# Performance work log

Hardware: AMD Instinct MI355X
Metric: run time of the kernel (lower is better)

Reference implementation:

```python
import jax, jax.numpy as jnp
import numpy as np

D = 512
H = 4
HD = D // H
FF = 4 * D
B = 512
T = 128
EMA_K = 128
LOC_K = 4
DECAY = 0.9
STEP = 0.5 / np.sqrt(128 / 32)  # 0.25
EPS = 1e-5


def layernorm(x, g, b):
    mu = jnp.mean(x, axis=-1, keepdims=True)
    var = jnp.mean(jnp.square(x - mu), axis=-1, keepdims=True)
    return (x - mu) * jax.lax.rsqrt(var + EPS) * g + b


def dwconv_causal(x, w):
    # x: (B,T,D), w: (D,K); torch Conv1d(groups=D, padding=K-1) sliced to [:T]
    K = w.shape[1]
    xt = jnp.transpose(x, (0, 2, 1))  # (B,D,T)
    y = jax.lax.conv_general_dilated(
        xt, w[:, None, :], window_strides=(1,), padding=[(K - 1, 0)],
        feature_group_count=x.shape[-1], dimension_numbers=('NCT', 'OIT', 'NCT'))
    return jnp.transpose(y, (0, 2, 1))


def rope(qk, cos, sin):
    # qk: (B,H,T,HD)
    x1, x2 = jnp.split(qk, 2, axis=-1)
    rot = jnp.concatenate([-x2, x1], axis=-1)
    return qk * cos + rot * sin


def setup_inputs() -> dict:
    key = jax.random.key(0)
    ks = jax.random.split(key, 24)
    s = 0.02
    inp = {
        'parallel_repr': jax.random.normal(ks[0], (B, T, D), jnp.float32),
        'sequential_state': jax.random.normal(ks[1], (B, D), jnp.float32),
        'q_w': jax.random.normal(ks[2], (D, D), jnp.float32) * s,
        'q_b': jnp.zeros((D,), jnp.float32),
        'k_w': jax.random.normal(ks[3], (D, D), jnp.float32) * s,
        'k_b': jnp.zeros((D,), jnp.float32),
        'v_w': jax.random.normal(ks[4], (D, D), jnp.float32) * s,
        'v_b': jnp.zeros((D,), jnp.float32),
        'o_w': jax.random.normal(ks[5], (D, D), jnp.float32) * s,
        'o_b': jnp.zeros((D,), jnp.float32),
        'local_w': jax.random.normal(ks[6], (D, LOC_K), jnp.float32) * 0.1,
        'local_b': jax.random.normal(ks[7], (D,), jnp.float32) * 0.1,
        'delta_w': jax.random.normal(ks[8], (3 * D, D), jnp.float32) * s,
        'delta_b': jnp.zeros((D,), jnp.float32),
        'gate_w': jax.random.normal(ks[9], (3 * D, D), jnp.float32) * s,
        'gate_b': jnp.zeros((D,), jnp.float32),
        'dn_g': jnp.ones((D,), jnp.float32), 'dn_b': jnp.zeros((D,), jnp.float32),
        'ln1_g': jnp.ones((D,), jnp.float32), 'ln1_b': jnp.zeros((D,), jnp.float32),
        'ln2_g': jnp.ones((D,), jnp.float32), 'ln2_b': jnp.zeros((D,), jnp.float32),
        'ln3_g': jnp.ones((D,), jnp.float32), 'ln3_b': jnp.zeros((D,), jnp.float32),
        'ln4_g': jnp.ones((D,), jnp.float32), 'ln4_b': jnp.zeros((D,), jnp.float32),
        'seq_w': jax.random.normal(ks[10], (D, D), jnp.float32) * s,
        'seq_b': jnp.zeros((D,), jnp.float32),
        'ffn_w1': jax.random.normal(ks[11], (D, FF), jnp.float32) * s,
        'ffn_b1': jnp.zeros((FF,), jnp.float32),
        'ffn_w2': jax.random.normal(ks[12], (FF, D), jnp.float32) * s,
        'ffn_b2': jnp.zeros((D,), jnp.float32),
    }
    # EMA kernel: coefficient (1-d)*d^lag on x[t-lag]; stored flipped as in torch
    ema = (1.0 - DECAY) * DECAY ** jnp.arange(EMA_K, dtype=jnp.float32)
    inp['ema_w'] = jnp.broadcast_to(ema[::-1][None, :], (D, EMA_K))
    return inp


def reference(parallel_repr, sequential_state, q_w, q_b, k_w, k_b, v_w, v_b,
              o_w, o_b, local_w, local_b, delta_w, delta_b, gate_w, gate_b,
              dn_g, dn_b, ln1_g, ln1_b, ln2_g, ln2_b, ln3_g, ln3_b, ln4_g, ln4_b,
              seq_w, seq_b, ffn_w1, ffn_b1, ffn_w2, ffn_b2, ema_w):
    x = parallel_repr
    Bb, Tt, Dd = x.shape
    # --- RoPE causal attention ---
    inv_freq = 1.0 / (10000.0 ** (jnp.arange(0, HD, 2, dtype=jnp.float32) / HD))
    t = jnp.arange(Tt, dtype=jnp.float32)
    freqs = jnp.outer(t, inv_freq)                      # (T, HD/2)
    emb = jnp.concatenate([freqs, freqs], axis=-1)      # (T, HD)
    cos = jnp.cos(emb)[None, None]
    sin = jnp.sin(emb)[None, None]
    def heads(y):
        return jnp.transpose(y.reshape(Bb, Tt, H, HD), (0, 2, 1, 3))
    q = rope(heads(x @ q_w + q_b), cos, sin)
    k = rope(heads(x @ k_w + k_b), cos, sin)
    v = heads(x @ v_w + v_b)
    scores = jnp.einsum('bhtd,bhsd->bhts', q, k) / np.sqrt(HD)
    causal = jnp.tril(jnp.ones((Tt, Tt), dtype=bool))
    scores = jnp.where(causal, scores, jnp.float32(-1e9))
    attn = jax.nn.softmax(scores, axis=-1)
    attn_out = jnp.einsum('bhts,bhsd->bhtd', attn, v)
    attn_out = jnp.transpose(attn_out, (0, 2, 1, 3)).reshape(Bb, Tt, Dd)
    attn_out = attn_out @ o_w + o_b
    x1 = layernorm(x + attn_out, ln1_g, ln1_b)
    # --- depthwise causal convs ---
    local_hist = dwconv_causal(x1, local_w) + local_b
    global_sum = dwconv_causal(x1, ema_w)
    combined = jnp.concatenate([x1, local_hist, global_sum], axis=-1)  # (B,T,3D)
    deltas = jax.nn.sigmoid(combined @ gate_w + gate_b) * jnp.tanh(combined @ delta_w + delta_b)
    deltas = layernorm(deltas, dn_g, dn_b)
    acc = jnp.cumsum(deltas, axis=1) * STEP
    states = layernorm(sequential_state[:, None, :] + acc, ln3_g, ln3_b)
    seq_guidance = states @ seq_w + seq_b
    ffn_in = x1 + 0.3 * seq_guidance
    h = jax.nn.gelu(ffn_in @ ffn_w1 + ffn_b1, approximate=False)
    ffn_out = h @ ffn_w2 + ffn_b2
    out = layernorm(x1 + ffn_out, ln2_g, ln2_b)
    final_state = layernorm(states[:, -1, :], ln4_g, ln4_b)
    return out, final_state
```

## Files before the change

### kernel.cpp

```cpp
#include <hip/hip_runtime.h>
#include <cstddef>
#include <cstdint>

#define BB   512
#define TT   128
#define DD   512
#define HH   4
#define HDIM 128
#define FFD  2048
#define NROWS (BB * TT)
#define SLOT ((size_t)NROWS * DD)

typedef unsigned short u16;
typedef __bf16 bf16x8 __attribute__((ext_vector_type(8)));
typedef float  f32x4  __attribute__((ext_vector_type(4)));

__device__ __forceinline__ u16 f2b(float x) {
    union { float f; unsigned u; } v; v.f = x;
    unsigned r = v.u + 0x7FFFu + ((v.u >> 16) & 1u);
    return (u16)(r >> 16);
}
__device__ __forceinline__ float b2f(u16 u) {
    union { unsigned u; float f; } v; v.u = (unsigned)u << 16; return v.f;
}
__device__ __forceinline__ float fast_gelu(float v) {
    float t = v * (0.7978845608028654f + 0.0356774081f * v * v);
    float e = __expf(2.f * t);
    float th = 1.f - 2.f / (e + 1.f);
    return 0.5f * v * (1.f + th);
}
__device__ __forceinline__ void glds16(const void* g, void* l) {
    __builtin_amdgcn_global_load_lds(
        (const __attribute__((address_space(1))) void*)g,
        (__attribute__((address_space(3))) void*)l, 16, 0, 0);
}

#define BAR() asm volatile("s_barrier" ::: "memory")
#define MM(ACC, AV, BV) \
    ACC = __builtin_amdgcn_mfma_f32_16x16x32_bf16(AV, BV, ACC, 0, 0, 0)

template<int MODE>
__global__ __launch_bounds__(512, 2)
void gemm256(const u16* __restrict__ A, const u16* __restrict__ BT,
             const float* __restrict__ bias, void* __restrict__ Cout, int ldc,
             const float* __restrict__ addsrc, int K, int M)
{
    __shared__ u16 S[65536];
    const int tid = threadIdx.x;
    const int gx  = gridDim.x;
    const int nwg = gx * gridDim.y;
    int orig = blockIdx.y * gx + blockIdx.x;
    orig = (orig & 7) * (nwg >> 3) + (orig >> 3);
    const int row0 = (orig / gx) * 256;
    const int col0 = (orig % gx) * 256;

    const int lane = tid & 63;
    const int wid  = tid >> 6;
    const int wm   = wid >> 2;
    const int wn   = wid & 3;
    const int fr   = lane & 15;
    const int kq   = lane >> 4;

    const int c0 = wid * 128 + lane;
    const int c1 = c0 + 64;
    const int l0 = c0 ^ (((c0 >> 5) & 1) << 1);
    const int l1 = c1 ^ (((c1 >> 5) & 1) << 1);
    const int sr0 = l0 >> 2, sk0 = (l0 & 3) * 8;
    const int sr1 = l1 >> 2, sk1 = (l1 & 3) * 8;
    const u16* ApG = A  + (size_t)row0 * K;
    const u16* BpG = BT + (size_t)col0 * K;

    auto stA = [&](int kt, int kh) {
        char* slot = (char*)S + ((((kt & 1) << 1) + kh) << 14);
        const u16* g = ApG + kt * 64 + kh * 32;
        glds16(g + (size_t)sr0 * K + sk0, slot + c0 * 16);
        glds16(g + (size_t)sr1 * K + sk1, slot + c1 * 16);
    };
    auto stB = [&](int kt, int kh) {
        char* slot = (char*)S + 65536 + ((((kt & 1) << 1) + kh) << 14);
        const u16* g = BpG + kt * 64 + kh * 32;
        glds16(g + (size_t)sr0 * K + sk0, slot + c0 * 16);
        glds16(g + (size_t)sr1 * K + sk1, slot + c1 * 16);
    };
    auto rdA = [&](int p, int kh, int m) -> bf16x8 {
        const int row = wm * 128 + m * 16 + fr;
        const int L = (row * 64 + kq * 16) ^ (((row >> 3) & 1) << 5);
        return *(const bf16x8*)((char*)S + (((p << 1) + kh) << 14) + L);
    };
    auto rdB = [&](int p, int kh, int n) -> bf16x8 {
        const int col = wn * 64 + n * 16 + fr;
        const int L = (col * 64 + kq * 16) ^ (((col >> 3) & 1) << 5);
        return *(const bf16x8*)((char*)S + 65536 + (((p << 1) + kh) << 14) + L);
    };

    f32x4 acc[8][4];
#pragma unroll
    for (int m = 0; m < 8; ++m)
#pragma unroll
        for (int n = 0; n < 4; ++n) acc[m][n] = (f32x4){0.f, 0.f, 0.f, 0.f};

    const int NKT = K >> 6;

    stA(0, 0); stA(0, 1); stB(0, 0); stB(0, 1);
    stB(1, 0); stB(1, 1); stA(1, 0);
    asm volatile("s_waitcnt vmcnt(6)" ::: "memory");
    BAR();

    for (int kt = 0; kt < NKT; ++kt) {
        const int p = kt & 1;
        const bool s1 = (kt + 1 < NKT);
        const bool s2 = (kt + 2 < NKT);
        bf16x8 a0, a1, a2, a3, a4, a5, a6, a7;
        bf16x8 b00, b01, b02, b03, b10, b11, b12, b13;

        if (s1) stA(kt + 1, 1);
        a0 = rdA(p, 0, 0); a1 = rdA(p, 0, 1); a2 = rdA(p, 0, 2); a3 = rdA(p, 0, 3);
        a4 = rdA(p, 1, 0); a5 = rdA(p, 1, 1); a6 = rdA(p, 1, 2); a7 = rdA(p, 1, 3);
        b00 = rdB(p, 0, 0); b01 = rdB(p, 0, 1);
        b10 = rdB(p, 1, 0); b11 = rdB(p, 1, 1);
        BAR();
        __builtin_amdgcn_s_setprio(1);
        MM(acc[0][0], a0, b00); MM(acc[0][1], a0, b01);
        MM(acc[1][0], a1, b00); MM(acc[1][1], a1, b01);
        MM(acc[2][0], a2, b00); MM(acc[2][1], a2, b01);
        MM(acc[3][0], a3, b00); MM(acc[3][1], a3, b01);
        MM(acc[0][0], a4, b10); MM(acc[0][1], a4, b11);
        MM(acc[1][0], a5, b10); MM(acc[1][1], a5, b11);
        MM(acc[2][0], a6, b10); MM(acc[2][1], a6, b11);
        MM(acc[3][0], a7, b10); MM(acc[3][1], a7, b11);
        __builtin_amdgcn_s_setprio(0);
        BAR();

        b02 = rdB(p, 0, 2); b03 = rdB(p, 0, 3);
        b12 = rdB(p, 1, 2); b13 = rdB(p, 1, 3);
        BAR();
        __builtin_amdgcn_s_setprio(1);
        MM(acc[0][2], a0, b02); MM(acc[0][3], a0, b03);
        MM(acc[1][2], a1, b02); MM(acc[1][3], a1, b03);
        MM(acc[2][2], a2, b02); MM(acc[2][3], a2, b03);
        MM(acc[3][2], a3, b02); MM(acc[3][3], a3, b03);
        MM(acc[0][2], a4, b12); MM(acc[0][3], a4, b13);
        MM(acc[1][2], a5, b12); MM(acc[1][3], a5, b13);
        MM(acc[2][2], a6, b12); MM(acc[2][3], a6, b13);
        MM(acc[3][2], a7, b12); MM(acc[3][3], a7, b13);
        __builtin_amdgcn_s_setprio(0);
        BAR();

        if (s2) stB(kt + 2, 0);
        a0 = rdA(p, 0, 4); a1 = rdA(p, 0, 5); a2 = rdA(p, 0, 6); a3 = rdA(p, 0, 7);
        a4 = rdA(p, 1, 4); a5 = rdA(p, 1, 5); a6 = rdA(p, 1, 6); a7 = rdA(p, 1, 7);
        BAR();
        __builtin_amdgcn_s_setprio(1);
        MM(acc[4][0], a0, b00); MM(acc[4][1], a0, b01);
        MM(acc[5][0], a1, b00); MM(acc[5][1], a1, b01);
        MM(acc[6][0], a2, b00); MM(acc[6][1], a2, b01);
        MM(acc[7][0], a3, b00); MM(acc[7][1], a3, b01);
        MM(acc[4][0], a4, b10); MM(acc[4][1], a4, b11);
        MM(acc[5][0], a5, b10); MM(acc[5][1], a5, b11);
        MM(acc[6][0], a6, b10); MM(acc[6][1], a6, b11);
        MM(acc[7][0], a7, b10); MM(acc[7][1], a7, b11);
        __builtin_amdgcn_s_setprio(0);
        BAR();

        if (s2) { stB(kt + 2, 1); stA(kt + 2, 0); }
        __builtin_amdgcn_s_setprio(1);
        MM(acc[4][2], a0, b02); MM(acc[4][3], a0, b03);
        MM(acc[5][2], a1, b02); MM(acc[5][3], a1, b03);
        MM(acc[6][2], a2, b02); MM(acc[6][3], a2, b03);
        MM(acc[7][2], a3, b02); MM(acc[7][3], a3, b03);
        MM(acc[4][2], a4, b12); MM(acc[4][3], a4, b13);
        MM(acc[5][2], a5, b12); MM(acc[5][3], a5, b13);
        MM(acc[6][2], a6, b12); MM(acc[6][3], a6, b13);
        MM(acc[7][2], a7, b12); MM(acc[7][3], a7, b13);
        __builtin_amdgcn_s_setprio(0);
        if (s2)      asm volatile("s_waitcnt vmcnt(6)" ::: "memory");
        else if (s1) asm volatile("s_waitcnt vmcnt(0)" ::: "memory");
        if (s1) BAR();
    }

#pragma unroll
    for (int m = 0; m < 8; ++m) {
#pragma unroll
        for (int jj = 0; jj < 4; ++jj) {
            const int r = row0 + wm * 128 + m * 16 + kq * 4 + jj;
#pragma unroll
            for (int n = 0; n < 4; ++n) {
                const int c = col0 + wn * 64 + n * 16 + fr;
                float v = acc[m][n][jj] + bias[c];
                if constexpr (MODE == 2) {
                    ((u16*)Cout)[(size_t)r * ldc + c] =
                        f2b(addsrc[(size_t)r * M + c] + 0.3f * v);
                } else if constexpr (MODE == 3) {
                    ((u16*)Cout)[(size_t)r * ldc + c] = f2b(fast_gelu(v));
                } else if constexpr (MODE == 6) {
                    float pth = __shfl_xor(v, 1);
                    if ((fr & 1) == 0) {
                        float sg = 1.f / (1.f + __expf(-v));
                        float e  = __expf(2.f * pth);
                        float th = 1.f - 2.f / (e + 1.f);
                        ((u16*)Cout)[(size_t)r * ldc + (c >> 1)] = f2b(sg * th);
                    }
                } else {
                    ((u16*)Cout)[(size_t)r * ldc + c] = f2b(v);
                }
            }
        }
    }
}

template<int MODE>
__global__ __launch_bounds__(256)
void gemm_bf16(const u16* __restrict__ A, const u16* __restrict__ BT,
               const float* __restrict__ bias, void* __restrict__ Cout, int ldc,
               const float* __restrict__ addsrc, void* __restrict__ aux,
               int K, int M)
{
    __shared__ u16 smem[16384];
    const int tid = threadIdx.x;
    const int gx  = gridDim.x;
    const int nwg = gx * gridDim.y;
    int orig = blockIdx.y * gx + blockIdx.x;
    if ((nwg & 7) == 0) orig = (orig & 7) * (nwg >> 3) + (orig >> 3);
    const int row0 = (orig / gx) * 128;
    const int col0 = (orig % gx) * 128;

    const int lane = tid & 63;
    const int w    = tid >> 6;
    const int wr   = (w >> 1) * 64;
    const int wc   = (w & 1) * 64;
    const int fr   = lane & 15;
    const int kg   = (lane >> 4) * 8;

    f32x4 acc[4][4];
#pragma unroll
    for (int m = 0; m < 4; ++m)
#pragma unroll
        for (int n = 0; n < 4; ++n) acc[m][n] = (f32x4){0.f, 0.f, 0.f, 0.f};

    const int srow = tid >> 2;
    const int skb  = (tid & 3) * 8;
    const u16* Ag = A  + (size_t)(row0 + srow) * K + skb;
    const u16* Bg = BT + (size_t)(col0 + srow) * K + skb;
    const int soff = srow * 32 + skb;

    auto stage = [&](int kt, int buf) {
        const int ko = kt * 32;
        u16* as = smem + buf * 8192 + soff;
        u16* bs = smem + buf * 8192 + 4096 + soff;
        glds16(Ag + ko,                  as);
        glds16(Ag + (size_t)64 * K + ko, as + 2048);
        glds16(Bg + ko,                  bs);
        glds16(Bg + (size_t)64 * K + ko, bs + 2048);
    };

    const int nk = K >> 5;
    stage(0, 0);
    for (int k = 0; k < nk; ++k) {
        if (k + 1 < nk) {
            stage(k + 1, (k + 1) & 1);
            asm volatile("s_waitcnt vmcnt(4)" ::: "memory");
        } else {
            asm volatile("s_waitcnt vmcnt(0)" ::: "memory");
        }
        __syncthreads();
        const u16* As = smem + (k & 1) * 8192;
        const u16* Bs = As + 4096;
        bf16x8 af[4], bfr[4];
#pragma unroll
        for (int m = 0; m < 4; ++m)
            af[m] = *reinterpret_cast<const bf16x8*>(&As[(wr + m * 16 + fr) * 32 + kg]);
#pragma unroll
        for (int n = 0; n < 4; ++n)
            bfr[n] = *reinterpret_cast<const bf16x8*>(&Bs[(wc + n * 16 + fr) * 32 + kg]);
#pragma unroll
        for (int m = 0; m < 4; ++m)
#pragma unroll
            for (int n = 0; n < 4; ++n)
                acc[m][n] = __builtin_amdgcn_mfma_f32_16x16x32_bf16(af[m], bfr[n], acc[m][n], 0, 0, 0);
        __syncthreads();
    }

    if constexpr (MODE == 7) {
        if (col0 >= 1024) {
#pragma unroll
            for (int m = 0; m < 4; ++m)
#pragma unroll
                for (int j = 0; j < 4; ++j) {
                    const int tl = wr + m * 16 + (lane >> 4) * 4 + j;
#pragma unroll
                    for (int n = 0; n < 4; ++n) {
                        const int dc = wc + n * 16 + fr;
                        float v = acc[m][n][j] + bias[col0 + dc];
                        *(u16*)((char*)smem + dc * 256 + ((tl * 2) ^ ((dc & 7) << 4))) = f2b(v);
                    }
                }
            __syncthreads();
            u16* dst = (u16*)aux + ((size_t)((row0 >> 7) * 4 + ((col0 - 1024) >> 7)) << 14);
#pragma unroll
            for (int i = 0; i < 8; ++i)
                *(uint4*)(dst + (size_t)(i * 256 + tid) * 8) =
                    *(const uint4*)((char*)smem + (size_t)(i * 256 + tid) * 16);
        } else {
#pragma unroll
            for (int m = 0; m < 4; ++m)
#pragma unroll
                for (int j = 0; j < 4; ++j) {
                    const int r = row0 + wr + m * 16 + (lane >> 4) * 4 + j;
#pragma unroll
                    for (int n = 0; n < 4; ++n) {
                        const int c = col0 + wc + n * 16 + fr;
                        ((u16*)Cout)[(size_t)r * 1024 + c] = f2b(acc[m][n][j] + bias[c]);
                    }
                }
        }
    }
    (void)ldc; (void)addsrc;
}

__global__ __launch_bounds__(256)
void wtrans_kernel(const float* __restrict__ W, u16* __restrict__ WT, int K, int M,
                   int rmul, int roff)
{
    __shared__ float t[32][33];
    const int m0 = blockIdx.x * 32;
    const int k0 = blockIdx.y * 32;
    const int tx = threadIdx.x;
    const int ty = threadIdx.y;
#pragma unroll
    for (int i = 0; i < 4; ++i) {
        int k = ty * 4 + i;
        t[k][tx] = W[(size_t)(k0 + k) * M + m0 + tx];
    }
    __syncthreads();
#pragma unroll
    for (int i = 0; i < 4; ++i) {
        int m = ty * 4 + i;
        WT[(size_t)((m0 + m) * rmul + roff) * K + k0 + tx] = f2b(t[tx][m]);
    }
}

__global__ void cast_f2b_kernel(const float* __restrict__ in, u16* __restrict__ out, size_t n4)
{
    size_t i = (size_t)blockIdx.x * blockDim.x + threadIdx.x;
    if (i >= n4) return;
    float4 v = reinterpret_cast<const float4*>(in)[i];
    union { u16 u[4]; uint2 d; } p;
    p.u[0] = f2b(v.x); p.u[1] = f2b(v.y); p.u[2] = f2b(v.z); p.u[3] = f2b(v.w);
    reinterpret_cast<uint2*>(out)[i] = p.d;
}

__global__ void rope_table_kernel(float* __restrict__ tabc, float* __restrict__ tabs)
{
    int idx = blockIdx.x * blockDim.x + threadIdx.x;
    if (idx >= TT * 64) return;
    int t = idx >> 6, j = idx & 63;
    float invf = expf(-(float)j * (9.210340371976184f / 64.f));
    float ang  = (float)t * invf;
    tabc[idx] = cosf(ang);
    tabs[idx] = sinf(ang);
}

__global__ void bias_build_kernel(const float* qb, const float* kb, const float* vb,
                                  const float* gb, const float* db,
                                  float* qkvb, float* gdb)
{
    int i = blockIdx.x * blockDim.x + threadIdx.x;
    if (i >= 512) return;
    qkvb[i] = qb[i]; qkvb[512 + i] = kb[i]; qkvb[1024 + i] = vb[i];
    gdb[2 * i] = gb[i]; gdb[2 * i + 1] = db[i];
}

__global__ __launch_bounds__(256)
void attn_mfma_kernel(const u16* __restrict__ QKg, const u16* __restrict__ VTg,
                      u16* __restrict__ Og,
                      const float* __restrict__ tabc, const float* __restrict__ tabs)
{
    __shared__ u16 SA[128 * 128];
    __shared__ u16 SB[128 * 128];
    const int h = blockIdx.x, b = blockIdx.y;
    const int tid  = threadIdx.x;
    const int lane = tid & 63;
    const int w    = tid >> 6;
    const int fr   = lane & 15;
    const int kq   = lane >> 4;
    const size_t baseq = ((size_t)(b * TT)) * 1024 + (size_t)h * HDIM;
    const size_t baseo = ((size_t)(b * TT)) * DD + (size_t)h * HDIM;

    {
        const int tg = tid >> 4;
        const int dg = tid & 15;
        const int j0 = (dg & 7) * 8;
        const bool hi = (dg & 8) != 0;
        for (int r = 0; r < 8; ++r) {
            const int t = r * 16 + tg;
            uint4 qv = *(const uint4*)(QKg + baseq + (size_t)t * 1024 + dg * 8);
            uint4 kv = *(const uint4*)(QKg + baseq + 512 + (size_t)t * 1024 + dg * 8);
            unsigned qa[4] = {qv.x, qv.y, qv.z, qv.w};
            unsigned ka[4] = {kv.x, kv.y, kv.z, kv.w};
            unsigned qb[4], kb[4];
#pragma unroll
            for (int i = 0; i < 4; ++i) {
                qb[i] = __shfl_xor((int)qa[i], 8);
                kb[i] = __shfl_xor((int)ka[i], 8);
            }
            const float* cp = tabc + t * 64 + j0;
            const float* sp = tabs + t * 64 + j0;
            u16 oq[8], ok[8];
#pragma unroll
            for (int e = 0; e < 8; ++e) {
                float fq = b2f((u16)(qa[e >> 1] >> ((e & 1) * 16)));
                float gq = b2f((u16)(qb[e >> 1] >> ((e & 1) * 16)));
                float fk = b2f((u16)(ka[e >> 1] >> ((e & 1) * 16)));
                float gk = b2f((u16)(kb[e >> 1] >> ((e & 1) * 16)));
                float c = cp[e], s = sp[e];
                oq[e] = f2b(hi ? fq * c + gq * s : fq * c - gq * s);
                ok[e] = f2b(hi ? fk * c + gk * s : fk * c - gk * s);
            }
            const int cb = (dg * 16) ^ ((t & 7) << 4);
            *(uint4*)((char*)SA + t * 256 + cb) = *(const uint4*)oq;
            *(uint4*)((char*)SB + t * 256 + cb) = *(const uint4*)ok;
        }
    }
    __syncthreads();

    f32x4 acc[2][8];
#pragma unroll
    for (int m = 0; m < 2; ++m)
#pragma unroll
        for (int n = 0; n < 8; ++n) acc[m][n] = (f32x4){0.f, 0.f, 0.f, 0.f};

    for (int k0 = 0; k0 < 128; k0 += 32) {
        const int cb = (k0 + kq * 8) * 2;
        bf16x8 af[2];
#pragma unroll
        for (int m = 0; m < 2; ++m) {
            const int row = w * 32 + m * 16 + fr;
            af[m] = *(const bf16x8*)((char*)SA + row * 256 + (cb ^ ((row & 7) << 4)));
        }
#pragma unroll
        for (int n = 0; n < 8; ++n) {
            const int row = n * 16 + fr;
            bf16x8 bf = *(const bf16x8*)((char*)SB + row * 256 + (cb ^ ((row & 7) << 4)));
            acc[0][n] = __builtin_amdgcn_mfma_f32_16x16x32_bf16(af[0], bf, acc[0][n], 0, 0, 0);
            acc[1][n] = __builtin_amdgcn_mfma_f32_16x16x32_bf16(af[1], bf, acc[1][n], 0, 0, 0);
        }
    }
    __syncthreads();

    {
        const u16* vsrc = VTg + ((size_t)(b * HH + h) << 14);
#pragma unroll
        for (int i = 0; i < 8; ++i)
            glds16(vsrc + (size_t)(i * 256 + tid) * 8,
                   SB + (size_t)(i * 256 + tid) * 8);
    }

    const float SC = 0.08838834764831845f;
#pragma unroll
    for (int m = 0; m < 2; ++m) {
#pragma unroll
        for (int j = 0; j < 4; ++j) {
            const int t = w * 32 + m * 16 + kq * 4 + j;
            float mx = -3.0e38f;
#pragma unroll
            for (int n = 0; n < 8; ++n) {
                const int s = n * 16 + fr;
                float v = acc[m][n][j];
                v = (s <= t) ? v * SC : -3.0e38f;
                acc[m][n][j] = v;
                mx = fmaxf(mx, v);
            }
            mx = fmaxf(mx, __shfl_xor(mx, 1));
            mx = fmaxf(mx, __shfl_xor(mx, 2));
            mx = fmaxf(mx, __shfl_xor(mx, 4));
            mx = fmaxf(mx, __shfl_xor(mx, 8));
            float sum = 0.f;
#pragma unroll
            for (int n = 0; n < 8; ++n) {
                float e = __expf(acc[m][n][j] - mx);
                acc[m][n][j] = e; sum += e;
            }
            sum += __shfl_xor(sum, 1); sum += __shfl_xor(sum, 2);
            sum += __shfl_xor(sum, 4); sum += __shfl_xor(sum, 8);
            const float inv = 1.f / sum;
#pragma unroll
            for (int n = 0; n < 8; ++n) {
                const int s = n * 16 + fr;
                *(u16*)((char*)SA + t * 256 + ((s * 2) ^ ((t & 7) << 4))) =
                    f2b(acc[m][n][j] * inv);
            }
        }
    }
    __syncthreads();

    f32x4 oa[2][8];
#pragma unroll
    for (int m = 0; m < 2; ++m)
#pragma unroll
        for (int n = 0; n < 8; ++n) oa[m][n] = (f32x4){0.f, 0.f, 0.f, 0.f};

    for (int k0 = 0; k0 < 128; k0 += 32) {
        const int cb = (k0 + kq * 8) * 2;
        bf16x8 pa[2];
#pragma unroll
        for (int m = 0; m < 2; ++m) {
            const int row = w * 32 + m * 16 + fr;
            pa[m] = *(const bf16x8*)((char*)SA + row * 256 + (cb ^ ((row & 7) << 4)));
        }
#pragma unroll
        for (int n = 0; n < 8; ++n) {
            const int row = n * 16 + fr;
            bf16x8 vb = *(const bf16x8*)((char*)SB + row * 256 + (cb ^ ((row & 7) << 4)));
            oa[0][n] = __builtin_amdgcn_mfma_f32_16x16x32_bf16(pa[0], vb, oa[0][n], 0, 0, 0);
            oa[1][n] = __builtin_amdgcn_mfma_f32_16x16x32_bf16(pa[1], vb, oa[1][n], 0, 0, 0);
        }
    }

#pragma unroll
    for (int m = 0; m < 2; ++m)
#pragma unroll
        for (int j = 0; j < 4; ++j) {
            const int t = w * 32 + m * 16 + kq * 4 + j;
            u16* orow = Og + baseo + (size_t)t * DD;
#pragma unroll
            for (int n = 0; n < 8; ++n)
                orow[n * 16 + fr] = f2b(oa[m][n][j]);
        }
}

__device__ __forceinline__ float2 blk_red512(float v, float (*red)[2], int tid)
{
    float s = v, ss = v * v;
#pragma unroll
    for (int off = 1; off < 64; off <<= 1) {
        s  += __shfl_xor(s, off);
        ss += __shfl_xor(ss, off);
    }
    if ((tid & 63) == 0) { red[tid >> 6][0] = s; red[tid >> 6][1] = ss; }
    __syncthreads();
    float S = 0.f, SS = 0.f;
#pragma unroll
    for (int w = 0; w < 8; ++w) { S += red[w][0]; SS += red[w][1]; }
    return make_float2(S, SS);
}

__global__ __launch_bounds__(512)
void ln1_chain_kernel(const float* __restrict__ x, const u16* __restrict__ oo,
                      const float* __restrict__ g, const float* __restrict__ bb,
                      const float* __restrict__ lw, const float* __restrict__ lb,
                      float* __restrict__ X1, u16* __restrict__ Cb)
{
    __shared__ float red[2][8][2];
    const int b = blockIdx.x, d = threadIdx.x;
    const float g_ = g[d], b_ = bb[d];
    const float w0 = lw[d * 4 + 0], w1 = lw[d * 4 + 1],
                w2 = lw[d * 4 + 2], w3 = lw[d * 4 + 3];
    const float lb_ = lb[d];
    const size_t rb = (size_t)b * TT;
    float h1 = 0.f, h2 = 0.f, h3 = 0.f, ema = 0.f;
    float v = x[(rb + 0) * DD + d] + b2f(oo[(rb + 0) * DD + d]);
    for (int t = 0; t < TT; ++t) {
        const int tn = (t < TT - 1) ? t + 1 : t;
        float vn = x[(rb + tn) * DD + d] + b2f(oo[(rb + tn) * DD + d]);
        float2 r = blk_red512(v, red[t & 1], d);
        float mu  = r.x * (1.f / DD);
        float var = r.y * (1.f / DD) - mu * mu;
        float x1v = (v - mu) * rsqrtf(var + 1e-5f) * g_ + b_;
        const size_t row = rb + t;
        X1[row * DD + d] = x1v;
        u16* crow = Cb + row * 1536;
        crow[d] = f2b(x1v);
        crow[512 + d]  = f2b(lb_ + w3 * x1v + w2 * h1 + w1 * h2 + w0 * h3);
        ema = 0.9f * ema + 0.1f * x1v;
        crow[1024 + d] = f2b(ema);
        h3 = h2; h2 = h1; h1 = x1v;
        v = vn;
    }
}

__global__ __launch_bounds__(512)
void state_chain_kernel(const u16* __restrict__ deltasB, const float* __restrict__ seqst,
                        const float* __restrict__ dng, const float* __restrict__ dnb,
                        const float* __restrict__ g3, const float* __restrict__ b3,
                        const float* __restrict__ g4, const float* __restrict__ b4,
                        u16* __restrict__ statesb, float* __restrict__ fstate)
{
    __shared__ float red[2][8][2];
    const int b = blockIdx.x, d = threadIdx.x;
    const float gd_ = dng[d], bd_ = dnb[d], g3_ = g3[d], b3_ = b3[d];
    const float seq = seqst[(size_t)b * DD + d];
    const size_t rb = (size_t)b * TT;
    float cum = 0.f;
    float v = b2f(deltasB[(rb + 0) * DD + d]);
    for (int t = 0; t < TT; ++t) {
        const int tn = (t < TT - 1) ? t + 1 : t;
        float vn = b2f(deltasB[(rb + tn) * DD + d]);
        float2 r0 = blk_red512(v, red[0], d);
        float mu  = r0.x * (1.f / DD);
        float var = r0.y * (1.f / DD) - mu * mu;
        float nd  = (v - mu) * rsqrtf(var + 1e-5f) * gd_ + bd_;
        cum += nd;
        float sv = seq + cum * 0.25f;
        float2 r1 = blk_red512(sv, red[1], d);
        mu  = r1.x * (1.f / DD);
        var = r1.y * (1.f / DD) - mu * mu;
        float o = (sv - mu) * rsqrtf(var + 1e-5f) * g3_ + b3_;
        statesb[(rb + t) * DD + d] = f2b(o);
        if (t == TT - 1) {
            float2 r2 = blk_red512(o, red[0], d);
            float mu4  = r2.x * (1.f / DD);
            float var4 = r2.y * (1.f / DD) - mu4 * mu4;
            fstate[(size_t)b * DD + d] = (o - mu4) * rsqrtf(var4 + 1e-5f) * g4[d] + b4[d];
        }
        v = vn;
    }
}

__global__ __launch_bounds__(256)
void ln2_kernel(const float* __restrict__ a, const u16* __restrict__ badd,
                const float* __restrict__ g, const float* __restrict__ bb,
                float* __restrict__ out)
{
    const int row = blockIdx.x;
    const int tid = threadIdx.x;
    const float* ap = a + (size_t)row * DD;
    const u16*   bp = badd + (size_t)row * DD;
    float v0 = ap[tid]       + b2f(bp[tid]);
    float v1 = ap[tid + 256] + b2f(bp[tid + 256]);
    float s  = v0 + v1;
    float ss = v0 * v0 + v1 * v1;
#pragma unroll
    for (int off = 1; off < 64; off <<= 1) {
        s  += __shfl_xor(s, off);
        ss += __shfl_xor(ss, off);
    }
    __shared__ float sm1[4], sm2[4];
    const int wid = tid >> 6;
    if ((tid & 63) == 0) { sm1[wid] = s; sm2[wid] = ss; }
    __syncthreads();
    s  = sm1[0] + sm1[1] + sm1[2] + sm1[3];
    ss = sm2[0] + sm2[1] + sm2[2] + sm2[3];
    const float mu  = s * (1.f / DD);
    const float var = ss * (1.f / DD) - mu * mu;
    const float r   = rsqrtf(var + 1e-5f);
    float* op = out + (size_t)row * DD;
    op[tid]       = (v0 - mu) * r * g[tid]       + bb[tid];
    op[tid + 256] = (v1 - mu) * r * g[tid + 256] + bb[tid + 256];
}

extern "C" void kernel_launch(void* const* d_in, const int* in_sizes, int n_in,
                              void* d_out, int out_size, void* d_ws, size_t ws_size,
                              hipStream_t stream)
{
    const float* x       = (const float*)d_in[0];
    const float* seqst   = (const float*)d_in[1];
    const float* q_w     = (const float*)d_in[2];
    const float* q_b     = (const float*)d_in[3];
    const float* k_w     = (const float*)d_in[4];
    const float* k_b     = (const float*)d_in[5];
    const float* v_w     = (const float*)d_in[6];
    const float* v_b     = (const float*)d_in[7];
    const float* o_w     = (const float*)d_in[8];
    const float* o_b     = (const float*)d_in[9];
    const float* local_w = (const float*)d_in[10];
    const float* local_b = (const float*)d_in[11];
    const float* delta_w = (const float*)d_in[12];
    const float* delta_b = (const float*)d_in[13];
    const float* gate_w  = (const float*)d_in[14];
    const float* gate_b  = (const float*)d_in[15];
    const float* dn_g    = (const float*)d_in[16];
    const float* dn_b    = (const float*)d_in[17];
    const float* ln1_g   = (const float*)d_in[18];
    const float* ln1_b   = (const float*)d_in[19];
    const float* ln2_g   = (const float*)d_in[20];
    const float* ln2_b   = (const float*)d_in[21];
    const float* ln3_g   = (const float*)d_in[22];
    const float* ln3_b   = (const float*)d_in[23];
    const float* ln4_g   = (const float*)d_in[24];
    const float* ln4_b   = (const float*)d_in[25];
    const float* seq_w   = (const float*)d_in[26];
    const float* seq_b   = (const float*)d_in[27];
    const float* ffn_w1  = (const float*)d_in[28];
    const float* ffn_b1  = (const float*)d_in[29];
    const float* ffn_w2  = (const float*)d_in[30];
    const float* ffn_b2  = (const float*)d_in[31];
    (void)in_sizes; (void)n_in; (void)out_size; (void)ws_size;

    float* out = (float*)d_out;
    char*  ws  = (char*)d_ws;
    const size_t MB = (size_t)1 << 20;

    u16*   xb      = (u16*)(ws + 0);
    u16*   QKb     = (u16*)(ws + 64 * MB);
    u16*   VTb     = (u16*)(ws + 192 * MB);
    u16*   attnb   = (u16*)(ws + 256 * MB);
    u16*   Oob     = (u16*)(ws + 0);
    u16*   Cb      = (u16*)(ws + 64 * MB);
    u16*   deltasB = (u16*)(ws + 256 * MB);
    u16*   statesb = (u16*)(ws + 320 * MB);
    u16*   ffn_inb = (u16*)(ws + 0);
    u16*   hb      = (u16*)(ws + 64 * MB);
    u16*   Fob     = (u16*)(ws + 320 * MB);
    u16*   WSq  = (u16*)(ws + 448 * MB);
    u16*   WSo  = (u16*)(ws + 450 * MB);
    u16*   WSgd = (u16*)(ws + 451 * MB);
    u16*   WSs  = (u16*)(ws + 455 * MB);
    u16*   WSf1 = (u16*)(ws + 456 * MB);
    u16*   WSf2 = (u16*)(ws + 458 * MB);
    float* qkvb = (float*)(ws + 460 * MB);
    float* gdb  = (float*)(ws + 461 * MB);

    float* X1     = out;
    float* tabc   = out + SLOT;
    float* tabs   = tabc + TT * 64;
    float* fstate = out + SLOT;

    const size_t NE = (size_t)NROWS * DD;

    rope_table_kernel<<<(TT * 64 + 255) / 256, 256, 0, stream>>>(tabc, tabs);
    cast_f2b_kernel<<<(unsigned)((NE / 4 + 255) / 256), 256, 0, stream>>>(x, xb, NE / 4);
    bias_build_kernel<<<2, 256, 0, stream>>>(q_b, k_b, v_b, gate_b, delta_b, qkvb, gdb);
    auto wt = [&](const float* W, u16* WT, int K, int M, int rmul, int roff) {
        wtrans_kernel<<<dim3(M / 32, K / 32), dim3(32, 8), 0, stream>>>(W, WT, K, M, rmul, roff);
    };
    wt(q_w, WSq, DD, DD, 1, 0);
    wt(k_w, WSq + (size_t)512 * DD, DD, DD, 1, 0);
    wt(v_w, WSq + (size_t)1024 * DD, DD, DD, 1, 0);
    wt(o_w, WSo, DD, DD, 1, 0);
    wt(gate_w,  WSgd, 3 * DD, DD, 2, 0);
    wt(delta_w, WSgd, 3 * DD, DD, 2, 1);
    wt(seq_w, WSs, DD, DD, 1, 0);
    wt(ffn_w1, WSf1, DD, FFD, 1, 0);
    wt(ffn_w2, WSf2, FFD, DD, 1, 0);

    gemm_bf16<7><<<dim3(12, 512), 256, 0, stream>>>(
        xb, WSq, qkvb, QKb, 1024, nullptr, VTb, DD, 1536);

    attn_mfma_kernel<<<dim3(HH, BB), 256, 0, stream>>>(QKb, VTb, attnb, tabc, tabs);

    gemm256<4><<<dim3(2, 256), 512, 0, stream>>>(
        attnb, WSo, o_b, Oob, DD, nullptr, DD, DD);

    ln1_chain_kernel<<<BB, 512, 0, stream>>>(x, Oob, ln1_g, ln1_b, local_w, local_b, X1, Cb);

    gemm256<6><<<dim3(4, 256), 512, 0, stream>>>(
        Cb, WSgd, gdb, deltasB, DD, nullptr, 3 * DD, 1024);

    state_chain_kernel<<<BB, 512, 0, stream>>>(
        deltasB, seqst, dn_g, dn_b, ln3_g, ln3_b, ln4_g, ln4_b, statesb, fstate);

    gemm256<2><<<dim3(2, 256), 512, 0, stream>>>(
        statesb, WSs, seq_b, ffn_inb, DD, X1, DD, DD);

    gemm256<3><<<dim3(8, 256), 512, 0, stream>>>(
        ffn_inb, WSf1, ffn_b1, hb, FFD, nullptr, DD, FFD);
    gemm256<4><<<dim3(2, 256), 512, 0, stream>>>(
        hb, WSf2, ffn_b2, Fob, DD, nullptr, FFD, DD);

    ln2_kernel<<<NROWS, 256, 0, stream>>>(X1, Fob, ln2_g, ln2_b, out);
}
```

Before: 1.655 ms.

## Drop fp32 X1 buffer, reuse bf16 copies, chunk FFN to keep hidden in cache

The LN1 chain now reads the bf16 input copy instead of fp32 x and no longer writes a separate fp32 X1 tensor. Later consumers (the seq-guidance residual and LN2) read x1 from the bf16 slice of the concatenated Cb buffer instead. The FFN is split into four row chunks so each chunk's 2048-wide hidden activation is smaller and may stay in the last-level cache between the two GEMMs. This cuts HBM traffic but adds bf16 rounding to the residual paths and a few more kernel launches.

New measurement: 1.778 ms. 7.4% more time.

```diff
diff --git a/kernel.cpp b/kernel.cpp
--- a/kernel.cpp
+++ b/kernel.cpp
@@ -43,7 +43,7 @@
 __global__ __launch_bounds__(512, 2)
 void gemm256(const u16* __restrict__ A, const u16* __restrict__ BT,
              const float* __restrict__ bias, void* __restrict__ Cout, int ldc,
-             const float* __restrict__ addsrc, int K, int M)
+             const u16* __restrict__ addsrc, int K, int M)
 {
     __shared__ u16 S[65536];
     const int tid = threadIdx.x;
@@ -188,8 +188,8 @@
                 const int c = col0 + wn * 64 + n * 16 + fr;
                 float v = acc[m][n][jj] + bias[c];
                 if constexpr (MODE == 2) {
-                    ((u16*)Cout)[(size_t)r * ldc + c] =
-                        f2b(addsrc[(size_t)r * M + c] + 0.3f * v);
+                    float xs = b2f(addsrc[(size_t)r * M + c]);
+                    ((u16*)Cout)[(size_t)r * ldc + c] = f2b(xs + 0.3f * v);
                 } else if constexpr (MODE == 3) {
                     ((u16*)Cout)[(size_t)r * ldc + c] = f2b(fast_gelu(v));
                 } else if constexpr (MODE == 6) {
@@ -545,10 +545,10 @@
 }
 
 __global__ __launch_bounds__(512)
-void ln1_chain_kernel(const float* __restrict__ x, const u16* __restrict__ oo,
+void ln1_chain_kernel(const u16* __restrict__ xb, const u16* __restrict__ oo,
                       const float* __restrict__ g, const float* __restrict__ bb,
                       const float* __restrict__ lw, const float* __restrict__ lb,
-                      float* __restrict__ X1, u16* __restrict__ Cb)
+                      u16* __restrict__ Cb)
 {
     __shared__ float red[2][8][2];
     const int b = blockIdx.x, d = threadIdx.x;
@@ -558,16 +558,15 @@
     const float lb_ = lb[d];
     const size_t rb = (size_t)b * TT;
     float h1 = 0.f, h2 = 0.f, h3 = 0.f, ema = 0.f;
-    float v = x[(rb + 0) * DD + d] + b2f(oo[(rb + 0) * DD + d]);
+    float v = b2f(xb[(rb + 0) * DD + d]) + b2f(oo[(rb + 0) * DD + d]);
     for (int t = 0; t < TT; ++t) {
         const int tn = (t < TT - 1) ? t + 1 : t;
-        float vn = x[(rb + tn) * DD + d] + b2f(oo[(rb + tn) * DD + d]);
+        float vn = b2f(xb[(rb + tn) * DD + d]) + b2f(oo[(rb + tn) * DD + d]);
         float2 r = blk_red512(v, red[t & 1], d);
         float mu  = r.x * (1.f / DD);
         float var = r.y * (1.f / DD) - mu * mu;
         float x1v = (v - mu) * rsqrtf(var + 1e-5f) * g_ + b_;
         const size_t row = rb + t;
-        X1[row * DD + d] = x1v;
         u16* crow = Cb + row * 1536;
         crow[d] = f2b(x1v);
         crow[512 + d]  = f2b(lb_ + w3 * x1v + w2 * h1 + w1 * h2 + w0 * h3);
@@ -617,16 +616,16 @@
 }
 
 __global__ __launch_bounds__(256)
-void ln2_kernel(const float* __restrict__ a, const u16* __restrict__ badd,
+void ln2_kernel(const u16* __restrict__ x1cb, const u16* __restrict__ fo,
                 const float* __restrict__ g, const float* __restrict__ bb,
                 float* __restrict__ out)
 {
     const int row = blockIdx.x;
     const int tid = threadIdx.x;
-    const float* ap = a + (size_t)row * DD;
-    const u16*   bp = badd + (size_t)row * DD;
-    float v0 = ap[tid]       + b2f(bp[tid]);
-    float v1 = ap[tid + 256] + b2f(bp[tid + 256]);
+    const u16* ap = x1cb + (size_t)row * 1536;
+    const u16* bp = fo   + (size_t)row * DD;
+    float v0 = b2f(ap[tid])       + b2f(bp[tid]);
+    float v1 = b2f(ap[tid + 256]) + b2f(bp[tid + 256]);
     float s  = v0 + v1;
     float ss = v0 * v0 + v1 * v1;
 #pragma unroll
@@ -694,12 +693,12 @@
     u16*   QKb     = (u16*)(ws + 64 * MB);
     u16*   VTb     = (u16*)(ws + 192 * MB);
     u16*   attnb   = (u16*)(ws + 256 * MB);
-    u16*   Oob     = (u16*)(ws + 0);
+    u16*   Oob     = (u16*)(ws + 320 * MB);
     u16*   Cb      = (u16*)(ws + 64 * MB);
     u16*   deltasB = (u16*)(ws + 256 * MB);
     u16*   statesb = (u16*)(ws + 320 * MB);
     u16*   ffn_inb = (u16*)(ws + 0);
-    u16*   hb      = (u16*)(ws + 64 * MB);
+    u16*   hb      = (u16*)(ws + 256 * MB);
     u16*   Fob     = (u16*)(ws + 320 * MB);
     u16*   WSq  = (u16*)(ws + 448 * MB);
     u16*   WSo  = (u16*)(ws + 450 * MB);
@@ -710,7 +709,6 @@
     float* qkvb = (float*)(ws + 460 * MB);
     float* gdb  = (float*)(ws + 461 * MB);
 
-    float* X1     = out;
     float* tabc   = out + SLOT;
     float* tabs   = tabc + TT * 64;
     float* fstate = out + SLOT;
@@ -741,7 +739,7 @@
     gemm256<4><<<dim3(2, 256), 512, 0, stream>>>(
         attnb, WSo, o_b, Oob, DD, nullptr, DD, DD);
 
-    ln1_chain_kernel<<<BB, 512, 0, stream>>>(x, Oob, ln1_g, ln1_b, local_w, local_b, X1, Cb);
+    ln1_chain_kernel<<<BB, 512, 0, stream>>>(xb, Oob, ln1_g, ln1_b, local_w, local_b, Cb);
 
     gemm256<6><<<dim3(4, 256), 512, 0, stream>>>(
         Cb, WSgd, gdb, deltasB, DD, nullptr, 3 * DD, 1024);
@@ -750,12 +748,19 @@
         deltasB, seqst, dn_g, dn_b, ln3_g, ln3_b, ln4_g, ln4_b, statesb, fstate);
 
     gemm256<2><<<dim3(2, 256), 512, 0, stream>>>(
-        statesb, WSs, seq_b, ffn_inb, DD, X1, DD, DD);
-
-    gemm256<3><<<dim3(8, 256), 512, 0, stream>>>(
-        ffn_inb, WSf1, ffn_b1, hb, FFD, nullptr, DD, FFD);
-    gemm256<4><<<dim3(2, 256), 512, 0, stream>>>(
-        hb, WSf2, ffn_b2, Fob, DD, nullptr, FFD, DD);
-
-    ln2_kernel<<<NROWS, 256, 0, stream>>>(X1, Fob, ln2_g, ln2_b, out);
-}
+        statesb, WSs, seq_b, ffn_inb, DD, Cb, DD, 1536);
+
+    {
+        const int CH = 16384;
+        for (int c = 0; c < 4; ++c) {
+            const u16* Ain = ffn_inb + (size_t)c * CH * DD;
+            u16* Cchunk    = Fob     + (size_t)c * CH * DD;
+            gemm256<3><<<dim3(8, CH / 256), 512, 0, stream>>>(
+                Ain, WSf1, ffn_b1, hb, FFD, nullptr, DD, FFD);
+            gemm256<4><<<dim3(2, CH / 256), 512, 0, stream>>>(
+                hb, WSf2, ffn_b2, Cchunk, DD, nullptr, FFD, DD);
+        }
+    }
+
+    ln2_kernel<<<NROWS, 256, 0, stream>>>(Cb, Fob, ln2_g, ln2_b, out);
+}
```
